# Performance work log

Hardware: AMD Instinct MI355X
Metric: run time of the kernel (lower is better)

Reference implementation:

```python
import jax, jax.numpy as jnp
import numpy as np

B = 64; H = 56; W = 56; C = 96; WS = 7; SHIFT = 3; NH = 3
N = WS * WS          # 49 tokens per window
NW = (H // WS) * (W // WS)  # 64 windows per image
HD = C // NH
MLP_H = 4 * C


def _rel_index():
    coords = np.stack(np.meshgrid(np.arange(WS), np.arange(WS), indexing='ij')).reshape(2, -1)
    rel = (coords[:, :, None] - coords[:, None, :]).transpose(1, 2, 0)
    rel[..., 0] += WS - 1
    rel[..., 1] += WS - 1
    rel[..., 0] *= 2 * WS - 1
    return rel.sum(-1)  # [N, N] int


def _attn_mask():
    img = np.zeros((H, W))
    cnt = 0
    sls = (slice(0, -WS), slice(-WS, -SHIFT), slice(-SHIFT, None))
    for hs in sls:
        for ws_ in sls:
            img[hs, ws_] = cnt
            cnt += 1
    mw = img.reshape(H // WS, WS, W // WS, WS).transpose(0, 2, 1, 3).reshape(-1, N)
    diff = mw[:, None, :] - mw[:, :, None]
    return np.where(diff != 0, -100.0, 0.0).astype(np.float32)  # [NW, N, N]


REL_IDX = jnp.asarray(_rel_index())
MASK = jnp.asarray(_attn_mask())


def _ln(x, g, b):
    mu = x.mean(-1, keepdims=True)
    var = ((x - mu) ** 2).mean(-1, keepdims=True)
    return (x - mu) * jax.lax.rsqrt(var + 1e-5) * g + b


def setup_inputs() -> dict:
    key = jax.random.key(0)
    ks = jax.random.split(key, 8)
    s = 0.02
    return {
        'x': jax.random.normal(ks[0], (B, H * W, C), jnp.float32),
        'norm1_g': jnp.ones((C,), jnp.float32),
        'norm1_b': jnp.zeros((C,), jnp.float32),
        'qkv_w': jax.random.normal(ks[1], (C, 3 * C), jnp.float32) * s,
        'qkv_b': jnp.zeros((3 * C,), jnp.float32),
        'proj_w': jax.random.normal(ks[2], (C, C), jnp.float32) * s,
        'proj_b': jnp.zeros((C,), jnp.float32),
        'rpb_table': jax.random.normal(ks[3], ((2 * WS - 1) ** 2, NH), jnp.float32) * s,
        'norm2_g': jnp.ones((C,), jnp.float32),
        'norm2_b': jnp.zeros((C,), jnp.float32),
        'fc1_w': jax.random.normal(ks[4], (C, MLP_H), jnp.float32) * s,
        'fc1_b': jnp.zeros((MLP_H,), jnp.float32),
        'fc2_w': jax.random.normal(ks[5], (MLP_H, C), jnp.float32) * s,
        'fc2_b': jnp.zeros((C,), jnp.float32),
    }


def reference(x, norm1_g, norm1_b, qkv_w, qkv_b, proj_w, proj_b, rpb_table,
              norm2_g, norm2_b, fc1_w, fc1_b, fc2_w, fc2_b):
    Bx = x.shape[0]
    shortcut = x
    h = _ln(x, norm1_g, norm1_b).reshape(Bx, H, W, C)
    # cyclic shift
    h = jnp.roll(h, (-SHIFT, -SHIFT), axis=(1, 2))
    # window partition -> [B*NW, N, C]
    win = h.reshape(Bx, H // WS, WS, W // WS, WS, C).transpose(0, 1, 3, 2, 4, 5).reshape(-1, N, C)
    B_ = win.shape[0]
    # qkv projection
    qkv = (win @ qkv_w + qkv_b).reshape(B_, N, 3, NH, HD).transpose(2, 0, 3, 1, 4)
    q, k, v = qkv[0], qkv[1], qkv[2]  # [B_, NH, N, HD]
    scale = HD ** -0.5
    attn = jnp.einsum('bhnd,bhmd->bhnm', q * scale, k)  # [B_, NH, N, N]
    bias = rpb_table[REL_IDX.reshape(-1)].reshape(N, N, NH).transpose(2, 0, 1)
    attn = attn + bias[None]
    # shifted-window mask
    attn = attn.reshape(Bx, NW, NH, N, N) + MASK[None, :, None]
    attn = jax.nn.softmax(attn.reshape(B_, NH, N, N), axis=-1)
    out = jnp.einsum('bhnm,bhmd->bnhd', attn, v).reshape(B_, N, C)
    out = out @ proj_w + proj_b
    # window reverse + reverse shift
    out = out.reshape(Bx, H // WS, W // WS, WS, WS, C).transpose(0, 1, 3, 2, 4, 5).reshape(Bx, H, W, C)
    out = jnp.roll(out, (SHIFT, SHIFT), axis=(1, 2)).reshape(Bx, H * W, C)
    x = shortcut + out
    # MLP
    h2 = _ln(x, norm2_g, norm2_b)
    h2 = jax.nn.gelu(h2 @ fc1_w + fc1_b, approximate=False) @ fc2_w + fc2_b
    return x + h2
```

## Files before the change

kernel.cpp:

```cpp
#include <hip/hip_runtime.h>
#include <hip/hip_bf16.h>
#include <math.h>

#define BB    64
#define HH    56
#define WW_   56
#define CC    96
#define WS    7
#define SHIFT 3
#define NHD   3
#define NT    49
#define NWIN  64
#define HD    32
#define MLPH  384
#define HWTOK (HH*WW_)
#define NTOK  (BB*HWTOK)
#define NWTOT (BB*NWIN)

#define IMG_S 10240
#define N_IMG 12
#define WS_NEED (16 + N_IMG*IMG_S*2)

typedef __attribute__((ext_vector_type(8))) short short8;
typedef __attribute__((ext_vector_type(4))) short short4v;
typedef __attribute__((ext_vector_type(4))) float floatx4;

__device__ __forceinline__ float b2fs(short s) {
    union { unsigned int u; float f; } cv;
    cv.u = ((unsigned int)(unsigned short)s) << 16;
    return cv.f;
}
__device__ __forceinline__ short f2b(float f) {
    union { __hip_bfloat16 h; short s; } cv;
    cv.h = __float2bfloat16(f);
    return cv.s;
}
__device__ __forceinline__ float ldv(const void* p, size_t i, bool bf) {
    return bf ? b2fs(((const short*)p)[i]) : ((const float*)p)[i];
}
__device__ __forceinline__ void stv(void* p, size_t i, bool bf, float v) {
    if (bf) ((short*)p)[i] = f2b(v);
    else    ((float*)p)[i] = v;
}
#define MFMA16(a,b,c) __builtin_amdgcn_mfma_f32_16x16x32_bf16((a),(b),(c),0,0,0)

__device__ __forceinline__ float gelu_f(float v) {
    float z  = v * 0.70710678118654752f;
    float az = fabsf(z);
    float t  = __fdividef(1.0f, fmaf(0.3275911f, az, 1.0f));
    float p  = fmaf(fmaf(fmaf(fmaf(1.061405429f, t, -1.453152027f), t,
                   1.421413741f), t, -0.284496736f), t, 0.254829592f) * t;
    float e  = __expf(-az*az);
    float er = fmaf(-p, e, 1.0f);
    er = (z < 0.f) ? -er : er;
    return 0.5f * v * (1.0f + er);
}

__global__ void dtype_probe(const void* __restrict__ n1g, int* __restrict__ flag) {
    if (threadIdx.x == 0) {
        float f = ((const float*)n1g)[0];
        *flag = (f == 1.0f) ? 0 : 1;
    }
}

__global__ void prep_kernel(
    const void* __restrict__ qkv_w, const void* __restrict__ proj_w,
    const void* __restrict__ fc1_w, const void* __restrict__ fc2_w,
    short* __restrict__ wimg, const int* __restrict__ flag)
{
    const bool bf = (*flag != 0);
    int idx = blockIdx.x * 256 + threadIdx.x;
    if (idx >= N_IMG*IMG_S) return;
    int img = idx / IMG_S, r = idx - img*IMG_S;
    short v = 0;
    if (r < 96*104) {
        int nc = r / 104, k = r - nc*104;
        if (k < 96) {
            float f;
            if (img < 3)       f = ldv(qkv_w, (size_t)k*(3*CC) + (nc>>5)*CC + img*HD + (nc&31), bf);
            else if (img == 3) f = ldv(proj_w, (size_t)k*CC + nc, bf);
            else if (img < 8)  f = ldv(fc1_w, (size_t)k*MLPH + (img-4)*96 + nc, bf);
            else               f = ldv(fc2_w, (size_t)((img-8)*96 + k)*CC + nc, bf);
            v = f2b(f);
        }
    }
    wimg[idx] = v;
}

__global__ __launch_bounds__(256, 4) void attn_pre2(
    const void* __restrict__ x,
    const void* __restrict__ n1g, const void* __restrict__ n1b,
    const void* __restrict__ qkv_b, const void* __restrict__ rpb,
    const void* __restrict__ proj_b,
    void* __restrict__ out, const int* __restrict__ flag,
    const short* __restrict__ wimg)
{
    __shared__ __attribute__((aligned(16))) short lx[64*104];
    __shared__ __attribute__((aligned(16))) short lqk[64*72];
    __shared__ __attribute__((aligned(16))) short lv[32*72];
    __shared__ __attribute__((aligned(16))) short lsm[64*72];
    __shared__ float lmu[64], lrs[64];
    __shared__ float lg[CC], lb[CC];
    short* lctx = lx;

    const bool bf = (*flag != 0);
    const int win = blockIdx.x;
    const int b   = win >> 6;
    const int wr  = win & 63;
    const int wh  = wr >> 3, ww = wr & 7;
    const int tid = threadIdx.x;
    const int lane = tid & 63;
    const int wv  = tid >> 6;
    const int c   = lane & 15;
    const int q   = lane >> 4;

    if (tid < CC) { lg[tid] = ldv(n1g, tid, bf); lb[tid] = ldv(n1b, tid, bf); }

    if (!bf) {
        const float* xf = (const float*)x;
        for (int idx = tid; idx < NT*24; idx += 256) {
            int n = idx / 24, c4 = idx - n*24;
            int i = n / WS, j = n - i*WS;
            int hg = wh*WS + i + SHIFT; if (hg >= HH)  hg -= HH;
            int wg = ww*WS + j + SHIFT; if (wg >= WW_) wg -= WW_;
            size_t t = (size_t)(b*HWTOK + hg*WW_ + wg);
            floatx4 v = *(const floatx4*)&xf[t*CC + c4*4];
            short4v s;
            s[0] = f2b(v[0]); s[1] = f2b(v[1]); s[2] = f2b(v[2]); s[3] = f2b(v[3]);
            *(short4v*)&lx[n*104 + c4*4] = s;
        }
    } else {
        for (int idx = tid; idx < NT*CC; idx += 256) {
            int n = idx / CC, cc_ = idx - n*CC;
            int i = n / WS, j = n - i*WS;
            int hg = wh*WS + i + SHIFT; if (hg >= HH)  hg -= HH;
            int wg = ww*WS + j + SHIFT; if (wg >= WW_) wg -= WW_;
            size_t t = (size_t)(b*HWTOK + hg*WW_ + wg);
            lx[n*104 + cc_] = f2b(ldv(x, t*CC + cc_, bf));
        }
    }
    for (int idx = tid; idx < 15*13; idx += 256) {
        int n = NT + idx/13, c8 = idx - (idx/13)*13;
        *(short8*)&lx[n*104 + c8*8] = (short8)0;
    }
    __syncthreads();

    {
        int t = tid >> 2, p = tid & 3;
        float s = 0.f, ss = 0.f;
        #pragma unroll
        for (int i = 0; i < 24; ++i) {
            float v = b2fs(lx[t*104 + p*24 + i]); s += v; ss += v*v;
        }
        s += __shfl_xor(s, 1); ss += __shfl_xor(ss, 1);
        s += __shfl_xor(s, 2); ss += __shfl_xor(ss, 2);
        if (p == 0) {
            float mu = s * (1.f/CC);
            float var = ss * (1.f/CC) - mu*mu;
            lmu[t] = mu; lrs[t] = rsqrtf(var + 1e-5f);
        }
    }
    __syncthreads();

    short8 af[3];
    #pragma unroll
    for (int kt = 0; kt < 3; ++kt) {
        int row = wv*16 + c;
        short8 raw = *(const short8*)&lx[row*104 + kt*32 + q*8];
        float mu = lmu[row], rs = lrs[row];
        short8 a;
        #pragma unroll
        for (int e = 0; e < 8; ++e) {
            int k = kt*32 + q*8 + e;
            a[e] = f2b((b2fs(raw[e]) - mu)*rs*lg[k] + lb[k]);
        }
        af[kt] = a;
    }

    const float scale = 0.17677669529663687f;

    for (int h = 0; h < NHD; ++h) {
        const short* bimg = wimg + h*IMG_S;

        floatx4 acc[6];
        #pragma unroll
        for (int nt = 0; nt < 6; ++nt) acc[nt] = (floatx4)0.f;
        #pragma unroll
        for (int kt = 0; kt < 3; ++kt) {
            #pragma unroll
            for (int nt = 0; nt < 6; ++nt) {
                short8 bfr = *(const short8*)&bimg[(nt*16 + c)*104 + kt*32 + q*8];
                acc[nt] = MFMA16(af[kt], bfr, acc[nt]);
            }
        }
        #pragma unroll
        for (int nt = 0; nt < 6; ++nt) {
            int ncol = nt*16 + c;
            int part = ncol >> 5, d = ncol & 31;
            float bias = ldv(qkv_b, part*CC + h*HD + d, bf);
            #pragma unroll
            for (int r = 0; r < 4; ++r) {
                int trow = wv*16 + q*4 + r;
                float v = acc[nt][r] + bias;
                if (part < 2) lqk[trow*72 + part*32 + d] = f2b(v);
                else          lv[d*72 + trow]            = f2b(v);
            }
        }
        __syncthreads();

        short8 aq = *(const short8*)&lqk[(wv*16 + c)*72 + q*8];
        floatx4 sv[4];
        #pragma unroll
        for (int nt = 0; nt < 4; ++nt) {
            short8 bk = *(const short8*)&lqk[(nt*16 + c)*72 + 32 + q*8];
            sv[nt] = MFMA16(aq, bk, (floatx4)0.f);
        }

        int ikA[4], jkA[4], rkA[4], tkA[4];
        #pragma unroll
        for (int nt = 0; nt < 4; ++nt) {
            int tk = nt*16 + c; tkA[nt] = tk;
            int ik = tk / 7, jk = tk - ik*7;
            ikA[nt] = ik; jkA[nt] = jk;
            int rh = (wh == 7) ? (ik < 4 ? 1 : 2) : 0;
            int rw = (ww == 7) ? (jk < 4 ? 1 : 2) : 0;
            rkA[nt] = rh*3 + rw;
        }
        #pragma unroll
        for (int r = 0; r < 4; ++r) {
            int tq = wv*16 + q*4 + r;
            int iq = tq / 7, jq = tq - iq*7;
            int rhq = (wh == 7) ? (iq < 4 ? 1 : 2) : 0;
            int rwq = (ww == 7) ? (jq < 4 ? 1 : 2) : 0;
            int rq = rhq*3 + rwq;
            float vals[4], mx = -1e30f;
            #pragma unroll
            for (int nt = 0; nt < 4; ++nt) {
                float v;
                if (tkA[nt] < NT) {
                    int rel = (iq - ikA[nt] + 6)*13 + (jq - jkA[nt] + 6);
                    rel = rel < 0 ? 0 : (rel > 168 ? 168 : rel);
                    v = sv[nt][r]*scale + ldv(rpb, rel*NHD + h, bf);
                    if (rkA[nt] != rq) v -= 100.f;
                } else v = -1e30f;
                vals[nt] = v; mx = fmaxf(mx, v);
            }
            mx = fmaxf(mx, __shfl_xor(mx, 1));
            mx = fmaxf(mx, __shfl_xor(mx, 2));
            mx = fmaxf(mx, __shfl_xor(mx, 4));
            mx = fmaxf(mx, __shfl_xor(mx, 8));
            float sum = 0.f;
            #pragma unroll
            for (int nt = 0; nt < 4; ++nt) { vals[nt] = __expf(vals[nt] - mx); sum += vals[nt]; }
            sum += __shfl_xor(sum, 1);
            sum += __shfl_xor(sum, 2);
            sum += __shfl_xor(sum, 4);
            sum += __shfl_xor(sum, 8);
            float inv = 1.f / sum;
            #pragma unroll
            for (int nt = 0; nt < 4; ++nt)
                lsm[(wv*16 + q*4 + r)*72 + nt*16 + c] = f2b(vals[nt]*inv);
        }
        floatx4 ov[2] = {(floatx4)0.f, (floatx4)0.f};
        #pragma unroll
        for (int kt = 0; kt < 2; ++kt) {
            short8 ap = *(const short8*)&lsm[(wv*16 + c)*72 + kt*32 + q*8];
            #pragma unroll
            for (int nt = 0; nt < 2; ++nt) {
                short8 bv = *(const short8*)&lv[(nt*16 + c)*72 + kt*32 + q*8];
                ov[nt] = MFMA16(ap, bv, ov[nt]);
            }
        }
        #pragma unroll
        for (int nt = 0; nt < 2; ++nt)
            #pragma unroll
            for (int r = 0; r < 4; ++r)
                lctx[(wv*16 + q*4 + r)*104 + h*HD + nt*16 + c] = f2b(ov[nt][r]);
        if (h < NHD-1) __syncthreads();
    }

    const short* pimg = wimg + 3*IMG_S;
    floatx4 po[6];
    #pragma unroll
    for (int nt = 0; nt < 6; ++nt) po[nt] = (floatx4)0.f;
    #pragma unroll
    for (int kt = 0; kt < 3; ++kt) {
        short8 ac = *(const short8*)&lctx[(wv*16 + c)*104 + kt*32 + q*8];
        #pragma unroll
        for (int nt = 0; nt < 6; ++nt) {
            short8 bp = *(const short8*)&pimg[(nt*16 + c)*104 + kt*32 + q*8];
            po[nt] = MFMA16(ac, bp, po[nt]);
        }
    }
    float pbv[6];
    #pragma unroll
    for (int nt = 0; nt < 6; ++nt) pbv[nt] = ldv(proj_b, nt*16 + c, bf);
    #pragma unroll
    for (int r = 0; r < 4; ++r) {
        int n = wv*16 + q*4 + r;
        if (n < NT) {
            int i = n / WS, j = n - i*WS;
            int hg = wh*WS + i + SHIFT; if (hg >= HH)  hg -= HH;
            int wg = ww*WS + j + SHIFT; if (wg >= WW_) wg -= WW_;
            size_t gbase = (size_t)(b*HWTOK + hg*WW_ + wg)*CC;
            #pragma unroll
            for (int nt = 0; nt < 6; ++nt) {
                size_t gi = gbase + nt*16 + c;
                stv(out, gi, bf, po[nt][r] + pbv[nt] + ldv(x, gi, bf));
            }
        }
    }
}

__global__ __launch_bounds__(256, 4) void mlp_pre4(
    void* __restrict__ out,
    const void* __restrict__ n2g, const void* __restrict__ n2b,
    const void* __restrict__ fc1_b, const void* __restrict__ fc2_b,
    const int* __restrict__ flag, const short* __restrict__ wimg)
{
    __shared__ __attribute__((aligned(16))) short lx1[64*104];
    __shared__ float lmu[64], lrs[64];
    __shared__ float lg[CC], lb[CC];
    short* lh = lx1;

    const bool bf = (*flag != 0);
    const int t0  = blockIdx.x * 64;
    const int tid = threadIdx.x;
    const int lane = tid & 63;
    const int wv  = tid >> 6;
    const int c   = lane & 15;
    const int q   = lane >> 4;

    if (tid < CC) { lg[tid] = ldv(n2g, tid, bf); lb[tid] = ldv(n2b, tid, bf); }
    if (!bf) {
        const float* of = (const float*)out;
        for (int idx = tid; idx < 64*24; idx += 256) {
            int n = idx / 24, c4 = idx - n*24;
            floatx4 v = *(const floatx4*)&of[(size_t)(t0+n)*CC + c4*4];
            short4v s;
            s[0] = f2b(v[0]); s[1] = f2b(v[1]); s[2] = f2b(v[2]); s[3] = f2b(v[3]);
            *(short4v*)&lx1[n*104 + c4*4] = s;
        }
    } else {
        for (int idx = tid; idx < 64*CC; idx += 256) {
            int n = idx / CC, cc_ = idx - n*CC;
            lx1[n*104 + cc_] = f2b(ldv(out, (size_t)(t0+n)*CC + cc_, bf));
        }
    }
    __syncthreads();

    {
        int t = tid >> 2, p = tid & 3;
        float s = 0.f, ss = 0.f;
        #pragma unroll
        for (int i = 0; i < 24; ++i) {
            float v = b2fs(lx1[t*104 + p*24 + i]); s += v; ss += v*v;
        }
        s += __shfl_xor(s, 1); ss += __shfl_xor(ss, 1);
        s += __shfl_xor(s, 2); ss += __shfl_xor(ss, 2);
        if (p == 0) {
            float mu = s * (1.f/CC);
            float var = ss * (1.f/CC) - mu*mu;
            lmu[t] = mu; lrs[t] = rsqrtf(var + 1e-5f);
        }
    }
    __syncthreads();

    short8 af[3];
    #pragma unroll
    for (int kt = 0; kt < 3; ++kt) {
        int row = wv*16 + c;
        short8 raw = *(const short8*)&lx1[row*104 + kt*32 + q*8];
        float mu = lmu[row], rs = lrs[row];
        short8 a;
        #pragma unroll
        for (int e = 0; e < 8; ++e) {
            int k = kt*32 + q*8 + e;
            a[e] = f2b((b2fs(raw[e]) - mu)*rs*lg[k] + lb[k]);
        }
        af[kt] = a;
    }
    __syncthreads();

    floatx4 acc2[6];
    #pragma unroll
    for (int nt = 0; nt < 6; ++nt) acc2[nt] = (floatx4)0.f;

    for (int qh = 0; qh < 4; ++qh) {
        const short* b1 = wimg + (4+qh)*IMG_S;
        #pragma unroll
        for (int nh = 0; nh < 2; ++nh) {
            floatx4 a1[3];
            #pragma unroll
            for (int nt2 = 0; nt2 < 3; ++nt2) a1[nt2] = (floatx4)0.f;
            #pragma unroll
            for (int kt = 0; kt < 3; ++kt) {
                #pragma unroll
                for (int nt2 = 0; nt2 < 3; ++nt2) {
                    int nt = nh*3 + nt2;
                    short8 bfr = *(const short8*)&b1[(nt*16 + c)*104 + kt*32 + q*8];
                    a1[nt2] = MFMA16(af[kt], bfr, a1[nt2]);
                }
            }
            #pragma unroll
            for (int nt2 = 0; nt2 < 3; ++nt2) {
                int nl = (nh*3 + nt2)*16 + c;
                float bias = ldv(fc1_b, qh*96 + nl, bf);
                #pragma unroll
                for (int r = 0; r < 4; ++r) {
                    float v = a1[nt2][r] + bias;
                    lh[(wv*16 + q*4 + r)*104 + nl] = f2b(gelu_f(v));
                }
            }
        }
        __syncthreads();

        const short* b2 = wimg + (8+qh)*IMG_S;
        #pragma unroll
        for (int kt = 0; kt < 3; ++kt) {
            short8 ah = *(const short8*)&lh[(wv*16 + c)*104 + kt*32 + q*8];
            #pragma unroll
            for (int nt = 0; nt < 6; ++nt) {
                short8 bw = *(const short8*)&b2[(nt*16 + c)*104 + kt*32 + q*8];
                acc2[nt] = MFMA16(ah, bw, acc2[nt]);
            }
        }
        __syncthreads();
    }

    float b2v[6];
    #pragma unroll
    for (int nt = 0; nt < 6; ++nt) b2v[nt] = ldv(fc2_b, nt*16 + c, bf);
    #pragma unroll
    for (int r = 0; r < 4; ++r) {
        int row = wv*16 + q*4 + r;
        size_t gbase = (size_t)(t0 + row)*CC;
        #pragma unroll
        for (int nt = 0; nt < 6; ++nt) {
            size_t gi = gbase + nt*16 + c;
            stv(out, gi, bf, acc2[nt][r] + b2v[nt] + ldv(out, gi, bf));
        }
    }
}

__global__ __launch_bounds__(256, 2) void attn_old(
    const void* __restrict__ x,
    const void* __restrict__ n1g, const void* __restrict__ n1b,
    const void* __restrict__ qkv_w, const void* __restrict__ qkv_b,
    const void* __restrict__ rpb,
    const void* __restrict__ proj_w, const void* __restrict__ proj_b,
    void* __restrict__ out, const int* __restrict__ flag)
{
    __shared__ __attribute__((aligned(16))) short lx[64*104];
    __shared__ __attribute__((aligned(16))) short lwb[96*104];
    __shared__ __attribute__((aligned(16))) short lqk[64*72];
    __shared__ __attribute__((aligned(16))) short lv[32*72];
    __shared__ __attribute__((aligned(16))) short lctx[64*104];
    __shared__ float lmu[64], lrs[64];
    __shared__ float lg[CC], lb[CC];
    short* lsm = lwb;

    const bool bf = (*flag != 0);
    const int win = blockIdx.x;
    const int b   = win >> 6;
    const int wr  = win & 63;
    const int wh  = wr >> 3, ww = wr & 7;
    const int tid = threadIdx.x;
    const int lane = tid & 63;
    const int wv  = tid >> 6;
    const int c   = lane & 15;
    const int q   = lane >> 4;

    if (tid < CC) { lg[tid] = ldv(n1g, tid, bf); lb[tid] = ldv(n1b, tid, bf); }

    for (int idx = tid; idx < NT*CC; idx += 256) {
        int n = idx / CC, cc_ = idx - n*CC;
        int i = n / WS, j = n - i*WS;
        int hg = wh*WS + i + SHIFT; if (hg >= HH)  hg -= HH;
        int wg = ww*WS + j + SHIFT; if (wg >= WW_) wg -= WW_;
        size_t t = (size_t)(b*HWTOK + hg*WW_ + wg);
        lx[n*104 + cc_] = f2b(ldv(x, t*CC + cc_, bf));
    }
    for (int idx = tid; idx < 15*CC; idx += 256) {
        int n = NT + idx/CC, cc_ = idx % CC;
        lx[n*104 + cc_] = 0;
    }
    __syncthreads();

    {
        int t = tid >> 2, p = tid & 3;
        float s = 0.f, ss = 0.f;
        #pragma unroll
        for (int i = 0; i < 24; ++i) {
            float v = b2fs(lx[t*104 + p*24 + i]); s += v; ss += v*v;
        }
        s += __shfl_xor(s, 1); ss += __shfl_xor(ss, 1);
        s += __shfl_xor(s, 2); ss += __shfl_xor(ss, 2);
        if (p == 0) {
            float mu = s * (1.f/CC);
            float var = ss * (1.f/CC) - mu*mu;
            lmu[t] = mu; lrs[t] = rsqrtf(var + 1e-5f);
        }
    }
    __syncthreads();
    for (int idx = tid; idx < NT*CC; idx += 256) {
        int n = idx / CC, cc_ = idx - n*CC;
        float v = b2fs(lx[n*104 + cc_]);
        lx[n*104 + cc_] = f2b((v - lmu[n]) * lrs[n] * lg[cc_] + lb[cc_]);
    }
    __syncthreads();

    const float scale = 0.17677669529663687f;

    for (int h = 0; h < NHD; ++h) {
        for (int idx = tid; idx < 96*96; idx += 256) {
            int k = idx / 96, nc = idx - (idx/96)*96;
            int part = nc >> 5, d = nc & 31;
            lwb[nc*104 + k] = f2b(ldv(qkv_w, (size_t)k*(3*CC) + part*CC + h*HD + d, bf));
        }
        __syncthreads();

        floatx4 acc[6];
        #pragma unroll
        for (int nt = 0; nt < 6; ++nt) acc[nt] = (floatx4)0.f;
        #pragma unroll
        for (int kt = 0; kt < 3; ++kt) {
            short8 af = *(const short8*)&lx[(wv*16 + c)*104 + kt*32 + q*8];
            #pragma unroll
            for (int nt = 0; nt < 6; ++nt) {
                short8 bfr = *(const short8*)&lwb[(nt*16 + c)*104 + kt*32 + q*8];
                acc[nt] = MFMA16(af, bfr, acc[nt]);
            }
        }
        #pragma unroll
        for (int nt = 0; nt < 6; ++nt) {
            int ncol = nt*16 + c;
            int part = ncol >> 5, d = ncol & 31;
            float bias = ldv(qkv_b, part*CC + h*HD + d, bf);
            #pragma unroll
            for (int r = 0; r < 4; ++r) {
                int trow = wv*16 + q*4 + r;
                float v = acc[nt][r] + bias;
                if (part < 2) lqk[trow*72 + part*32 + d] = f2b(v);
                else          lv[d*72 + trow]            = f2b(v);
            }
        }
        __syncthreads();

        short8 aq = *(const short8*)&lqk[(wv*16 + c)*72 + q*8];
        floatx4 sv[4];
        #pragma unroll
        for (int nt = 0; nt < 4; ++nt) {
            short8 bk = *(const short8*)&lqk[(nt*16 + c)*72 + 32 + q*8];
            sv[nt] = MFMA16(aq, bk, (floatx4)0.f);
        }

        int ikA[4], jkA[4], rkA[4], tkA[4];
        #pragma unroll
        for (int nt = 0; nt < 4; ++nt) {
            int tk = nt*16 + c; tkA[nt] = tk;
            int ik = tk / 7, jk = tk - ik*7;
            ikA[nt] = ik; jkA[nt] = jk;
            int rh = (wh == 7) ? (ik < 4 ? 1 : 2) : 0;
            int rw = (ww == 7) ? (jk < 4 ? 1 : 2) : 0;
            rkA[nt] = rh*3 + rw;
        }
        #pragma unroll
        for (int r = 0; r < 4; ++r) {
            int tq = wv*16 + q*4 + r;
            int iq = tq / 7, jq = tq - iq*7;
            int rhq = (wh == 7) ? (iq < 4 ? 1 : 2) : 0;
            int rwq = (ww == 7) ? (jq < 4 ? 1 : 2) : 0;
            int rq = rhq*3 + rwq;
            float vals[4], mx = -1e30f;
            #pragma unroll
            for (int nt = 0; nt < 4; ++nt) {
                float v;
                if (tkA[nt] < NT) {
                    int rel = (iq - ikA[nt] + 6)*13 + (jq - jkA[nt] + 6);
                    rel = rel < 0 ? 0 : (rel > 168 ? 168 : rel);
                    v = sv[nt][r]*scale + ldv(rpb, rel*NHD + h, bf);
                    if (rkA[nt] != rq) v -= 100.f;
                } else v = -1e30f;
                vals[nt] = v; mx = fmaxf(mx, v);
            }
            mx = fmaxf(mx, __shfl_xor(mx, 1));
            mx = fmaxf(mx, __shfl_xor(mx, 2));
            mx = fmaxf(mx, __shfl_xor(mx, 4));
            mx = fmaxf(mx, __shfl_xor(mx, 8));
            float sum = 0.f;
            #pragma unroll
            for (int nt = 0; nt < 4; ++nt) { vals[nt] = __expf(vals[nt] - mx); sum += vals[nt]; }
            sum += __shfl_xor(sum, 1);
            sum += __shfl_xor(sum, 2);
            sum += __shfl_xor(sum, 4);
            sum += __shfl_xor(sum, 8);
            float inv = 1.f / sum;
            #pragma unroll
            for (int nt = 0; nt < 4; ++nt)
                lsm[(wv*16 + q*4 + r)*72 + nt*16 + c] = f2b(vals[nt]*inv);
        }
        floatx4 ov[2] = {(floatx4)0.f, (floatx4)0.f};
        #pragma unroll
        for (int kt = 0; kt < 2; ++kt) {
            short8 ap = *(const short8*)&lsm[(wv*16 + c)*72 + kt*32 + q*8];
            #pragma unroll
            for (int nt = 0; nt < 2; ++nt) {
                short8 bv = *(const short8*)&lv[(nt*16 + c)*72 + kt*32 + q*8];
                ov[nt] = MFMA16(ap, bv, ov[nt]);
            }
        }
        #pragma unroll
        for (int nt = 0; nt < 2; ++nt)
            #pragma unroll
            for (int r = 0; r < 4; ++r)
                lctx[(wv*16 + q*4 + r)*104 + h*HD + nt*16 + c] = f2b(ov[nt][r]);
        __syncthreads();
    }

    for (int idx = tid; idx < 96*96; idx += 256) {
        int k = idx / 96, nc = idx - (idx/96)*96;
        lwb[nc*104 + k] = f2b(ldv(proj_w, (size_t)k*CC + nc, bf));
    }
    __syncthreads();

    floatx4 po[6];
    #pragma unroll
    for (int nt = 0; nt < 6; ++nt) po[nt] = (floatx4)0.f;
    #pragma unroll
    for (int kt = 0; kt < 3; ++kt) {
        short8 ac = *(const short8*)&lctx[(wv*16 + c)*104 + kt*32 + q*8];
        #pragma unroll
        for (int nt = 0; nt < 6; ++nt) {
            short8 bp = *(const short8*)&lwb[(nt*16 + c)*104 + kt*32 + q*8];
            po[nt] = MFMA16(ac, bp, po[nt]);
        }
    }
    #pragma unroll
    for (int nt = 0; nt < 6; ++nt) {
        int ncol = nt*16 + c;
        float bias = ldv(proj_b, ncol, bf);
        #pragma unroll
        for (int r = 0; r < 4; ++r) {
            int n = wv*16 + q*4 + r;
            if (n < NT) {
                int i = n / WS, j = n - i*WS;
                int hg = wh*WS + i + SHIFT; if (hg >= HH)  hg -= HH;
                int wg = ww*WS + j + SHIFT; if (wg >= WW_) wg -= WW_;
                size_t t = (size_t)(b*HWTOK + hg*WW_ + wg);
                stv(out, t*CC + ncol, bf, po[nt][r] + bias + ldv(x, t*CC + ncol, bf));
            }
        }
    }
}

__global__ __launch_bounds__(256, 3) void mlp_old(
    void* __restrict__ out,
    const void* __restrict__ n2g, const void* __restrict__ n2b,
    const void* __restrict__ fc1_w, const void* __restrict__ fc1_b,
    const void* __restrict__ fc2_w, const void* __restrict__ fc2_b,
    const int* __restrict__ flag)
{
    __shared__ __attribute__((aligned(16))) short lx1[64*104];
    __shared__ __attribute__((aligned(16))) short lh[64*104];
    __shared__ __attribute__((aligned(16))) short lw[96*104];
    __shared__ float lmu[64], lrs[64];
    __shared__ float lg[CC], lb[CC];

    const bool bf = (*flag != 0);
    const int t0  = blockIdx.x * 64;
    const int tid = threadIdx.x;
    const int lane = tid & 63;
    const int wv  = tid >> 6;
    const int c   = lane & 15;
    const int q   = lane >> 4;

    if (tid < CC) { lg[tid] = ldv(n2g, tid, bf); lb[tid] = ldv(n2b, tid, bf); }
    for (int idx = tid; idx < 64*CC; idx += 256) {
        int n = idx / CC, cc_ = idx - n*CC;
        lx1[n*104 + cc_] = f2b(ldv(out, (size_t)(t0+n)*CC + cc_, bf));
    }
    __syncthreads();

    {
        int t = tid >> 2, p = tid & 3;
        float s = 0.f, ss = 0.f;
        #pragma unroll
        for (int i = 0; i < 24; ++i) {
            float v = b2fs(lx1[t*104 + p*24 + i]); s += v; ss += v*v;
        }
        s += __shfl_xor(s, 1); ss += __shfl_xor(ss, 1);
        s += __shfl_xor(s, 2); ss += __shfl_xor(ss, 2);
        if (p == 0) {
            float mu = s * (1.f/CC);
            float var = ss * (1.f/CC) - mu*mu;
            lmu[t] = mu; lrs[t] = rsqrtf(var + 1e-5f);
        }
    }
    __syncthreads();

    short8 af[3];
    #pragma unroll
    for (int kt = 0; kt < 3; ++kt) {
        int row = wv*16 + c;
        short8 raw = *(const short8*)&lx1[row*104 + kt*32 + q*8];
        float mu = lmu[row], rs = lrs[row];
        short8 a;
        #pragma unroll
        for (int e = 0; e < 8; ++e) {
            int k = kt*32 + q*8 + e;
            a[e] = f2b((b2fs(raw[e]) - mu)*rs*lg[k] + lb[k]);
        }
        af[kt] = a;
    }

    floatx4 acc2[6];
    #pragma unroll
    for (int nt = 0; nt < 6; ++nt) acc2[nt] = (floatx4)0.f;

    for (int qh = 0; qh < 4; ++qh) {
        for (int idx = tid; idx < 96*96; idx += 256) {
            int k = idx / 96, nl = idx - (idx/96)*96;
            lw[nl*104 + k] = f2b(ldv(fc1_w, (size_t)k*MLPH + qh*96 + nl, bf));
        }
        __syncthreads();

        floatx4 a1[6];
        #pragma unroll
        for (int nt = 0; nt < 6; ++nt) a1[nt] = (floatx4)0.f;
        #pragma unroll
        for (int kt = 0; kt < 3; ++kt) {
            #pragma unroll
            for (int nt = 0; nt < 6; ++nt) {
                short8 bfr = *(const short8*)&lw[(nt*16 + c)*104 + kt*32 + q*8];
                a1[nt] = MFMA16(af[kt], bfr, a1[nt]);
            }
        }
        #pragma unroll
        for (int nt = 0; nt < 6; ++nt) {
            int nl = nt*16 + c;
            float bias = ldv(fc1_b, qh*96 + nl, bf);
            #pragma unroll
            for (int r = 0; r < 4; ++r) {
                float v = a1[nt][r] + bias;
                float g = 0.5f*v*(1.f + erff(v*0.70710678118654752f));
                lh[(wv*16 + q*4 + r)*104 + nl] = f2b(g);
            }
        }
        __syncthreads();

        for (int idx = tid; idx < 96*96; idx += 256) {
            int kl = idx / 96, n = idx - (idx/96)*96;
            lw[n*104 + kl] = f2b(ldv(fc2_w, (size_t)(qh*96 + kl)*CC + n, bf));
        }
        __syncthreads();

        #pragma unroll
        for (int kt = 0; kt < 3; ++kt) {
            short8 ah = *(const short8*)&lh[(wv*16 + c)*104 + kt*32 + q*8];
            #pragma unroll
            for (int nt = 0; nt < 6; ++nt) {
                short8 bw = *(const short8*)&lw[(nt*16 + c)*104 + kt*32 + q*8];
                acc2[nt] = MFMA16(ah, bw, acc2[nt]);
            }
        }
        __syncthreads();
    }

    #pragma unroll
    for (int nt = 0; nt < 6; ++nt) {
        int ncol = nt*16 + c;
        float bias = ldv(fc2_b, ncol, bf);
        #pragma unroll
        for (int r = 0; r < 4; ++r) {
            int row = wv*16 + q*4 + r;
            size_t gi = (size_t)(t0 + row)*CC + ncol;
            stv(out, gi, bf, acc2[nt][r] + bias + ldv(out, gi, bf));
        }
    }
}

__global__ void mfma_probe(void* __restrict__ out, const int* __restrict__ flag) {
    __shared__ float A[16*32];
    __shared__ float Bm[32*16];
    __shared__ __attribute__((aligned(16))) short As[16*104];
    __shared__ int lf1[64], lf2[64];

    const bool bfm = (*flag != 0);
    const int tid = threadIdx.x;
    for (int i = tid; i < 16*32; i += 64) {
        int m = i >> 5, k = i & 31;
        A[i] = (float)((m*7 + k*3) % 11 - 5) * 0.125f;
    }
    for (int i = tid; i < 32*16; i += 64) {
        int k = i >> 4, n = i & 15;
        Bm[i] = (float)((k*5 + n*2) % 13 - 6) * 0.0625f;
    }
    __syncthreads();
    for (int i = tid; i < 16*32; i += 64) {
        int m = i >> 5, k = i & 31;
        As[m*104 + k] = f2b(A[i]);
    }
    __syncthreads();

    const int c = tid & 15, q = tid >> 4;
    short8 a, b;
    #pragma unroll
    for (int j = 0; j < 8; ++j) {
        a[j] = f2b(A[c*32 + q*8 + j]);
        b[j] = f2b(Bm[(q*8 + j)*16 + c]);
    }
    short8 av = *(const short8*)&As[c*104 + q*8];
    int f2 = 0;
    #pragma unroll
    for (int j = 0; j < 8; ++j) if (av[j] != a[j]) f2 = 1;

    floatx4 acc = (floatx4)0.f;
    acc = MFMA16(a, b, acc);
    int f1 = 0;
    #pragma unroll
    for (int r = 0; r < 4; ++r) {
        float ref = 0.f;
        for (int k = 0; k < 32; ++k)
            ref += b2fs(f2b(A[(q*4 + r)*32 + k])) * b2fs(f2b(Bm[k*16 + c]));
        float d = fabsf(acc[r] - ref);
        if (!(d <= 0.02f)) f1 = 1;
    }
    lf1[tid] = f1; lf2[tid] = f2;
    __syncthreads();

    if (tid == 0) {
        int any1 = 0, any2 = 0;
        for (int i = 0; i < 64; ++i) { any1 |= lf1[i]; any2 |= lf2[i]; }
        float pert = any1 ? 0.06f : 0.f;
        float tiny = 0.f;
        if (any2) {
            float s = 1.0001f;
            for (int i = 0; i < 400000; ++i) s = s * 0.9999999f + 1e-9f;
            tiny = s * 1e-38f;
        }
        stv(out, 0, bfm, ldv(out, 0, bfm) + pert + tiny);
    }
}

extern "C" void kernel_launch(void* const* d_in, const int* in_sizes, int n_in,
                              void* d_out, int out_size, void* d_ws, size_t ws_size,
                              hipStream_t stream) {
    const void* x      = d_in[0];
    const void* n1g    = d_in[1];
    const void* n1b    = d_in[2];
    const void* qkv_w  = d_in[3];
    const void* qkv_b  = d_in[4];
    const void* proj_w = d_in[5];
    const void* proj_b = d_in[6];
    const void* rpb    = d_in[7];
    const void* n2g    = d_in[8];
    const void* n2b    = d_in[9];
    const void* fc1_w  = d_in[10];
    const void* fc1_b  = d_in[11];
    const void* fc2_w  = d_in[12];
    const void* fc2_b  = d_in[13];
    int* flag = (int*)d_ws;

    hipLaunchKernelGGL(dtype_probe, dim3(1), dim3(64), 0, stream, n1g, flag);

    if (ws_size >= (size_t)WS_NEED) {
        short* wimg = (short*)((char*)d_ws + 16);
        hipLaunchKernelGGL(prep_kernel, dim3((N_IMG*IMG_S + 255)/256), dim3(256), 0, stream,
                           qkv_w, proj_w, fc1_w, fc2_w, wimg, flag);
        hipLaunchKernelGGL(attn_pre2, dim3(NWTOT), dim3(256), 0, stream,
                           x, n1g, n1b, qkv_b, rpb, proj_b, d_out, flag, wimg);
        hipLaunchKernelGGL(mlp_pre4, dim3(NTOK/64), dim3(256), 0, stream,
                           d_out, n2g, n2b, fc1_b, fc2_b, flag, wimg);
    } else {
        hipLaunchKernelGGL(attn_old, dim3(NWTOT), dim3(256), 0, stream,
                           x, n1g, n1b, qkv_w, qkv_b, rpb, proj_w, proj_b, d_out, flag);
        hipLaunchKernelGGL(mlp_old, dim3(NTOK/64), dim3(256), 0, stream,
                           d_out, n2g, n2b, fc1_w, fc1_b, fc2_w, fc2_b, flag);
    }
    hipLaunchKernelGGL(mfma_probe, dim3(1), dim3(64), 0, stream, d_out, flag);
}
```

Baseline: 526.4 us.

## Process 128 tokens per MLP block with per-wave private rows, drop block barriers

New measurement: 489.3 us. -7.1%, faster.

```diff
diff --git a/kernel.cpp b/kernel.cpp
--- a/kernel.cpp
+++ b/kernel.cpp
@@ -312,94 +312,101 @@
     }
 }
 
-__global__ __launch_bounds__(256, 4) void mlp_pre4(
+__global__ __launch_bounds__(256, 2) void mlp_x2(
     void* __restrict__ out,
     const void* __restrict__ n2g, const void* __restrict__ n2b,
     const void* __restrict__ fc1_b, const void* __restrict__ fc2_b,
     const int* __restrict__ flag, const short* __restrict__ wimg)
 {
-    __shared__ __attribute__((aligned(16))) short lx1[64*104];
-    __shared__ float lmu[64], lrs[64];
+    __shared__ __attribute__((aligned(16))) short lx1[128*104];
+    __shared__ float lmu[128], lrs[128];
     __shared__ float lg[CC], lb[CC];
     short* lh = lx1;
 
     const bool bf = (*flag != 0);
-    const int t0  = blockIdx.x * 64;
+    const int t0  = blockIdx.x * 128;
     const int tid = threadIdx.x;
     const int lane = tid & 63;
     const int wv  = tid >> 6;
+    const int rb  = wv * 32;
     const int c   = lane & 15;
     const int q   = lane >> 4;
 
     if (tid < CC) { lg[tid] = ldv(n2g, tid, bf); lb[tid] = ldv(n2b, tid, bf); }
+
     if (!bf) {
         const float* of = (const float*)out;
-        for (int idx = tid; idx < 64*24; idx += 256) {
+        for (int idx = lane; idx < 32*24; idx += 64) {
             int n = idx / 24, c4 = idx - n*24;
-            floatx4 v = *(const floatx4*)&of[(size_t)(t0+n)*CC + c4*4];
+            floatx4 v = *(const floatx4*)&of[(size_t)(t0+rb+n)*CC + c4*4];
             short4v s;
             s[0] = f2b(v[0]); s[1] = f2b(v[1]); s[2] = f2b(v[2]); s[3] = f2b(v[3]);
-            *(short4v*)&lx1[n*104 + c4*4] = s;
+            *(short4v*)&lx1[(rb+n)*104 + c4*4] = s;
         }
     } else {
-        for (int idx = tid; idx < 64*CC; idx += 256) {
+        for (int idx = lane; idx < 32*CC; idx += 64) {
             int n = idx / CC, cc_ = idx - n*CC;
-            lx1[n*104 + cc_] = f2b(ldv(out, (size_t)(t0+n)*CC + cc_, bf));
-        }
-    }
-    __syncthreads();
+            lx1[(rb+n)*104 + cc_] = f2b(ldv(out, (size_t)(t0+rb+n)*CC + cc_, bf));
+        }
+    }
 
     {
-        int t = tid >> 2, p = tid & 3;
+        int tr = rb + (lane >> 1), p = lane & 1;
         float s = 0.f, ss = 0.f;
         #pragma unroll
-        for (int i = 0; i < 24; ++i) {
-            float v = b2fs(lx1[t*104 + p*24 + i]); s += v; ss += v*v;
+        for (int i = 0; i < 48; ++i) {
+            float v = b2fs(lx1[tr*104 + p*48 + i]); s += v; ss += v*v;
         }
         s += __shfl_xor(s, 1); ss += __shfl_xor(ss, 1);
-        s += __shfl_xor(s, 2); ss += __shfl_xor(ss, 2);
         if (p == 0) {
             float mu = s * (1.f/CC);
             float var = ss * (1.f/CC) - mu*mu;
-            lmu[t] = mu; lrs[t] = rsqrtf(var + 1e-5f);
-        }
-    }
-    __syncthreads();
-
-    short8 af[3];
-    #pragma unroll
-    for (int kt = 0; kt < 3; ++kt) {
-        int row = wv*16 + c;
-        short8 raw = *(const short8*)&lx1[row*104 + kt*32 + q*8];
-        float mu = lmu[row], rs = lrs[row];
-        short8 a;
-        #pragma unroll
-        for (int e = 0; e < 8; ++e) {
-            int k = kt*32 + q*8 + e;
-            a[e] = f2b((b2fs(raw[e]) - mu)*rs*lg[k] + lb[k]);
-        }
-        af[kt] = a;
-    }
-    __syncthreads();
-
-    floatx4 acc2[6];
-    #pragma unroll
-    for (int nt = 0; nt < 6; ++nt) acc2[nt] = (floatx4)0.f;
+            lmu[tr] = mu; lrs[tr] = rsqrtf(var + 1e-5f);
+        }
+    }
+    __syncthreads();
+
+    short8 af[2][3];
+    #pragma unroll
+    for (int tt = 0; tt < 2; ++tt) {
+        #pragma unroll
+        for (int kt = 0; kt < 3; ++kt) {
+            int row = rb + tt*16 + c;
+            short8 raw = *(const short8*)&lx1[row*104 + kt*32 + q*8];
+            float mu = lmu[row], rs = lrs[row];
+            short8 a;
+            #pragma unroll
+            for (int e = 0; e < 8; ++e) {
+                int k = kt*32 + q*8 + e;
+                a[e] = f2b((b2fs(raw[e]) - mu)*rs*lg[k] + lb[k]);
+            }
+            af[tt][kt] = a;
+        }
+    }
+
+    floatx4 acc2[2][6];
+    #pragma unroll
+    for (int tt = 0; tt < 2; ++tt)
+        #pragma unroll
+        for (int nt = 0; nt < 6; ++nt) acc2[tt][nt] = (floatx4)0.f;
 
     for (int qh = 0; qh < 4; ++qh) {
         const short* b1 = wimg + (4+qh)*IMG_S;
         #pragma unroll
         for (int nh = 0; nh < 2; ++nh) {
-            floatx4 a1[3];
-            #pragma unroll
-            for (int nt2 = 0; nt2 < 3; ++nt2) a1[nt2] = (floatx4)0.f;
+            floatx4 a1[2][3];
+            #pragma unroll
+            for (int tt = 0; tt < 2; ++tt)
+                #pragma unroll
+                for (int nt2 = 0; nt2 < 3; ++nt2) a1[tt][nt2] = (floatx4)0.f;
             #pragma unroll
             for (int kt = 0; kt < 3; ++kt) {
                 #pragma unroll
                 for (int nt2 = 0; nt2 < 3; ++nt2) {
                     int nt = nh*3 + nt2;
                     short8 bfr = *(const short8*)&b1[(nt*16 + c)*104 + kt*32 + q*8];
-                    a1[nt2] = MFMA16(af[kt], bfr, a1[nt2]);
+                    a1[0][nt2] = MFMA16(af[0][kt], bfr, a1[0][nt2]);
+                    a1[1][nt2] = MFMA16(af[1][kt], bfr, a1[1][nt2]);
                 }
             }
             #pragma unroll
@@ -407,9 +414,12 @@
                 int nl = (nh*3 + nt2)*16 + c;
                 float bias = ldv(fc1_b, qh*96 + nl, bf);
                 #pragma unroll
-                for (int r = 0; r < 4; ++r) {
-                    float v = a1[nt2][r] + bias;
-                    lh[(wv*16 + q*4 + r)*104 + nl] = f2b(gelu_f(v));
+                for (int tt = 0; tt < 2; ++tt) {
+                    #pragma unroll
+                    for (int r = 0; r < 4; ++r) {
+                        float v = a1[tt][nt2][r] + bias;
+                        lh[(rb + tt*16 + q*4 + r)*104 + nl] = f2b(gelu_f(v));
+                    }
                 }
             }
         }
@@ -418,27 +428,31 @@
         const short* b2 = wimg + (8+qh)*IMG_S;
         #pragma unroll
         for (int kt = 0; kt < 3; ++kt) {
-            short8 ah = *(const short8*)&lh[(wv*16 + c)*104 + kt*32 + q*8];
+            short8 ah0 = *(const short8*)&lh[(rb + c)*104 + kt*32 + q*8];
+            short8 ah1 = *(const short8*)&lh[(rb + 16 + c)*104 + kt*32 + q*8];
             #pragma unroll
             for (int nt = 0; nt < 6; ++nt) {
                 short8 bw = *(const short8*)&b2[(nt*16 + c)*104 + kt*32 + q*8];
-                acc2[nt] = MFMA16(ah, bw, acc2[nt]);
-            }
-        }
-        __syncthreads();
+                acc2[0][nt] = MFMA16(ah0, bw, acc2[0][nt]);
+                acc2[1][nt] = MFMA16(ah1, bw, acc2[1][nt]);
+            }
+        }
     }
 
     float b2v[6];
     #pragma unroll
     for (int nt = 0; nt < 6; ++nt) b2v[nt] = ldv(fc2_b, nt*16 + c, bf);
     #pragma unroll
-    for (int r = 0; r < 4; ++r) {
-        int row = wv*16 + q*4 + r;
-        size_t gbase = (size_t)(t0 + row)*CC;
-        #pragma unroll
-        for (int nt = 0; nt < 6; ++nt) {
-            size_t gi = gbase + nt*16 + c;
-            stv(out, gi, bf, acc2[nt][r] + b2v[nt] + ldv(out, gi, bf));
+    for (int tt = 0; tt < 2; ++tt) {
+        #pragma unroll
+        for (int r = 0; r < 4; ++r) {
+            int row = rb + tt*16 + q*4 + r;
+            size_t gbase = (size_t)(t0 + row)*CC;
+            #pragma unroll
+            for (int nt = 0; nt < 6; ++nt) {
+                size_t gi = gbase + nt*16 + c;
+                stv(out, gi, bf, acc2[tt][nt][r] + b2v[nt] + ldv(out, gi, bf));
+            }
         }
     }
 }
@@ -870,7 +884,7 @@
                            qkv_w, proj_w, fc1_w, fc2_w, wimg, flag);
         hipLaunchKernelGGL(attn_pre2, dim3(NWTOT), dim3(256), 0, stream,
                            x, n1g, n1b, qkv_b, rpb, proj_b, d_out, flag, wimg);
-        hipLaunchKernelGGL(mlp_pre4, dim3(NTOK/64), dim3(256), 0, stream,
+        hipLaunchKernelGGL(mlp_x2, dim3(NTOK/128), dim3(256), 0, stream,
                            d_out, n2g, n2b, fc1_b, fc2_b, flag, wimg);
     } else {
         hipLaunchKernelGGL(attn_old, dim3(NWTOT), dim3(256), 0, stream,
```
